# Performance work log

Measured on AMD Instinct MI355X. Metric: run time of the kernel, lower is better.

Reference implementation:

```python
import jax, jax.numpy as jnp
import numpy as np
from jax import lax

DROP_PROB = 0.1
BLOCK_SIZE = 7
B, C, H, W = 64, 256, 56, 56
HM, WM = H - (BLOCK_SIZE - 1), W - (BLOCK_SIZE - 1)


def setup_inputs() -> dict:
    key = jax.random.key(0)
    k1, k2 = jax.random.split(key)
    x = jax.random.normal(k1, (B, C, H, W), dtype=jnp.float32)
    mask_u = jax.random.uniform(k2, (B, C, HM, WM), dtype=jnp.float32)
    return {"x": x, "mask_u": mask_u}


def reference(x, mask_u):
    bs = BLOCK_SIZE
    feat = x.shape[2]
    # gamma as in _compute_gamma
    gamma = DROP_PROB / bs**2 * feat**2 / (feat - bs + 1) ** 2
    # Bernoulli(gamma) sample, deterministic given mask_u
    mask = (mask_u < gamma).astype(x.dtype)  # (B,C,HM,WM)
    # The nonzero/scatter block expansion in the original is exactly a
    # stride-1 max-pool with a bs x bs window and (bs-1, bs-1) zero padding,
    # producing the (B,C,H,W) padded dropped-region mask.
    blocked = lax.reduce_window(
        mask, 0.0, lax.max,
        window_dimensions=(1, 1, bs, bs),
        window_strides=(1, 1, 1, 1),
        padding=((0, 0), (0, 0), (bs - 1, bs - 1), (bs - 1, bs - 1)),
    )
    block_mask = 1.0 - blocked  # (B,C,H,W)
    scale = block_mask.size / block_mask.sum()
    return x * block_mask * scale
```

## Files before the change

kernel.cpp:

```cpp
#include <hip/hip_runtime.h>


#define BB 64
#define CC 256
#define HH 56
#define WW 56
#define HMM 50
#define WMM 50
#define BS 7

static constexpr unsigned int NPLANE = BB * CC;
static constexpr unsigned int NTOT   = BB * CC * HH * WW;
static constexpr unsigned int NV     = NTOT / 4;

__global__ void __launch_bounds__(256) dropblock_mask_kernel(
    const float* __restrict__ mask_u,
    unsigned long long* __restrict__ rowmask,
    unsigned int* __restrict__ plane_cnt,
    float gamma)
{
    const unsigned int wid   = threadIdx.x >> 6;
    const unsigned int lane  = threadIdx.x & 63u;
    const unsigned int plane = blockIdx.x * 4u + wid;
    const float* mu = mask_u + (size_t)plane * (HMM * WMM);

    unsigned long long my_d = 0ull;

    #pragma unroll
    for (int i = 0; i < HMM; ++i) {
        float v = (lane < WMM) ? mu[i * WMM + lane] : 1.0f;
        unsigned long long m = __ballot(v < gamma);
        unsigned long long d = m | (m << 1);
        d |= d << 2;
        d |= d << 3;
        if (lane == (unsigned)i) my_d = d;
    }

    unsigned long long blocked = my_d;
    blocked |= __shfl_up(blocked, 1, 64);
    blocked |= __shfl_up(blocked, 2, 64);
    blocked |= __shfl_up(blocked, 3, 64);

    if (lane < HH) rowmask[plane * HH + lane] = blocked;

    unsigned int cnt = __popcll(blocked);
    #pragma unroll
    for (int off = 32; off > 0; off >>= 1)
        cnt += __shfl_down(cnt, off, 64);
    if (lane == 0) plane_cnt[plane] = cnt;
}

__global__ void __launch_bounds__(1024) dropblock_scale_kernel(
    const unsigned int* __restrict__ plane_cnt,
    float* __restrict__ scale_out)
{
    __shared__ unsigned int ssum[16];
    const unsigned int t = threadIdx.x;

    const uint4* pc4 = reinterpret_cast<const uint4*>(plane_cnt);
    uint4 a = pc4[t];
    uint4 b = pc4[t + 1024];
    uint4 c = pc4[t + 2048];
    uint4 d = pc4[t + 3072];
    unsigned int s = a.x + a.y + a.z + a.w
                   + b.x + b.y + b.z + b.w
                   + c.x + c.y + c.z + c.w
                   + d.x + d.y + d.z + d.w;

    #pragma unroll
    for (int off = 32; off > 0; off >>= 1)
        s += __shfl_down(s, off, 64);
    if ((t & 63u) == 0u) ssum[t >> 6] = s;
    __syncthreads();

    if (t < 16) {
        unsigned int v = ssum[t];
        #pragma unroll
        for (int off = 8; off > 0; off >>= 1)
            v += __shfl_down(v, off, 64);
        if (t == 0) {
            *scale_out = (float)NTOT / (float)(NTOT - v);
        }
    }
}

__global__ void __launch_bounds__(256) dropblock_apply_kernel(
    const float* __restrict__ x,
    const unsigned long long* __restrict__ rowmask,
    const float* __restrict__ scale_ptr,
    float* __restrict__ out)
{
    unsigned int idx = blockIdx.x * 256u + threadIdx.x;
    if (idx >= NV) return;

    const float scale = *scale_ptr;

    unsigned int plane = idx / (HH * WW / 4);
    unsigned int rem   = idx - plane * (HH * WW / 4);
    unsigned int row   = rem / (WW / 4);
    unsigned int colv  = rem - row * (WW / 4);
    unsigned int col   = colv * 4;

    unsigned long long rm = rowmask[plane * HH + row];
    float4 xv = reinterpret_cast<const float4*>(x)[idx];
    float4 o;
    o.x = ((rm >> (col + 0)) & 1ull) ? 0.0f : xv.x * scale;
    o.y = ((rm >> (col + 1)) & 1ull) ? 0.0f : xv.y * scale;
    o.z = ((rm >> (col + 2)) & 1ull) ? 0.0f : xv.z * scale;
    o.w = ((rm >> (col + 3)) & 1ull) ? 0.0f : xv.w * scale;
    reinterpret_cast<float4*>(out)[idx] = o;
}

extern "C" void kernel_launch(void* const* d_in, const int* in_sizes, int n_in,
                              void* d_out, int out_size, void* d_ws, size_t ws_size,
                              hipStream_t stream) {
    const float* x      = (const float*)d_in[0];
    const float* mask_u = (const float*)d_in[1];
    float* out          = (float*)d_out;

    float* scale_ws             = (float*)d_ws;
    unsigned int* plane_cnt     = (unsigned int*)((char*)d_ws + 64);
    unsigned long long* rowmask = (unsigned long long*)((char*)d_ws + 65600);

    const double gd = 0.1 / ((double)BS * BS) * ((double)HH * HH) /
                      (((double)HH - BS + 1.0) * ((double)HH - BS + 1.0));
    const float gamma = (float)gd;

    dropblock_mask_kernel<<<NPLANE / 4, 256, 0, stream>>>(
        mask_u, rowmask, plane_cnt, gamma);

    dropblock_scale_kernel<<<1, 1024, 0, stream>>>(plane_cnt, scale_ws);

    dropblock_apply_kernel<<<(NV + 255u) / 256u, 256, 0, stream>>>(
        x, rowmask, scale_ws, out);
}
```

Measured before the change: 454.8 us.

## Stage mask_u through LDS with coalesced float4 prefetch, 16 planes per block

The mask kernel now loads four planes at a time into shared memory using coalesced float4 loads and register double-buffering. The next group of four planes is prefetched while the current one is processed with ballots. Each block handles 16 planes and writes one per-block count, so the scale kernel reduces 1024 values instead of 16384. This replaces strided 50-float row loads with fully vectorized streaming, at the cost of higher register and LDS use per block and lower parallelism in the mask kernel.

Result: faster. 440.5 us (-3.1%).

```diff
diff --git a/kernel.cpp b/kernel.cpp
--- a/kernel.cpp
+++ b/kernel.cpp
@@ -9,78 +9,114 @@
 #define WMM 50
 #define BS 7
 
-static constexpr unsigned int NPLANE = BB * CC;
-static constexpr unsigned int NTOT   = BB * CC * HH * WW;
-static constexpr unsigned int NV     = NTOT / 4;
+static constexpr unsigned int NPLANE  = BB * CC;
+static constexpr unsigned int NTOT    = BB * CC * HH * WW;
+static constexpr unsigned int NV      = NTOT / 4;
+static constexpr unsigned int PLANEF  = HMM * WMM;
+static constexpr unsigned int PLANE4  = PLANEF / 4;
+static constexpr unsigned int MGRID   = 1024;
+static constexpr unsigned int MPPB    = 16;
+static constexpr unsigned int MROUNDS = 4;
+static constexpr unsigned int R4CNT   = 4 * PLANE4;
+
+typedef float f32x4 __attribute__((ext_vector_type(4)));
 
 __global__ void __launch_bounds__(256) dropblock_mask_kernel(
     const float* __restrict__ mask_u,
     unsigned long long* __restrict__ rowmask,
-    unsigned int* __restrict__ plane_cnt,
+    unsigned int* __restrict__ block_cnt,
     float gamma)
 {
-    const unsigned int wid   = threadIdx.x >> 6;
-    const unsigned int lane  = threadIdx.x & 63u;
-    const unsigned int plane = blockIdx.x * 4u + wid;
-    const float* mu = mask_u + (size_t)plane * (HMM * WMM);
+    const unsigned int tid  = threadIdx.x;
+    const unsigned int wid  = tid >> 6;
+    const unsigned int lane = tid & 63u;
+    const unsigned int b    = blockIdx.x;
 
-    unsigned long long my_d = 0ull;
+    __shared__ float4 lds4[R4CNT];
+    __shared__ unsigned int csh[4];
+    const float* lds = reinterpret_cast<const float*>(lds4);
 
+    const float4* base = reinterpret_cast<const float4*>(mask_u)
+                       + (size_t)b * (MPPB * PLANE4);
+
+    float4 pf[10];
     #pragma unroll
-    for (int i = 0; i < HMM; ++i) {
-        float v = (lane < WMM) ? mu[i * WMM + lane] : 1.0f;
-        unsigned long long m = __ballot(v < gamma);
-        unsigned long long d = m | (m << 1);
-        d |= d << 2;
-        d |= d << 3;
-        if (lane == (unsigned)i) my_d = d;
+    for (unsigned int s = 0; s < 10; ++s) {
+        unsigned int i = tid + s * 256u;
+        pf[s] = (i < R4CNT) ? base[i] : make_float4(0.f, 0.f, 0.f, 0.f);
     }
 
-    unsigned long long blocked = my_d;
-    blocked |= __shfl_up(blocked, 1, 64);
-    blocked |= __shfl_up(blocked, 2, 64);
-    blocked |= __shfl_up(blocked, 3, 64);
+    unsigned int wcnt = 0;
 
-    if (lane < HH) rowmask[plane * HH + lane] = blocked;
+    for (unsigned int r = 0; r < MROUNDS; ++r) {
+        #pragma unroll
+        for (unsigned int s = 0; s < 10; ++s) {
+            unsigned int i = tid + s * 256u;
+            if (i < R4CNT) lds4[i] = pf[s];
+        }
+        __syncthreads();
 
-    unsigned int cnt = __popcll(blocked);
-    #pragma unroll
-    for (int off = 32; off > 0; off >>= 1)
-        cnt += __shfl_down(cnt, off, 64);
-    if (lane == 0) plane_cnt[plane] = cnt;
+        if (r + 1 < MROUNDS) {
+            const float4* src = base + (r + 1) * R4CNT;
+            #pragma unroll
+            for (unsigned int s = 0; s < 10; ++s) {
+                unsigned int i = tid + s * 256u;
+                pf[s] = (i < R4CNT) ? src[i] : make_float4(0.f, 0.f, 0.f, 0.f);
+            }
+        }
+
+        const float* mu = lds + wid * PLANEF;
+        unsigned long long my_d = 0ull;
+        #pragma unroll
+        for (int i = 0; i < HMM; ++i) {
+            float v = (lane < WMM) ? mu[i * WMM + lane] : 1.0f;
+            unsigned long long m = __ballot(v < gamma);
+            unsigned long long d = m | (m << 1);
+            d |= d << 2;
+            d |= d << 3;
+            if (lane == (unsigned)i) my_d = d;
+        }
+        unsigned long long blocked = my_d;
+        blocked |= __shfl_up(blocked, 1, 64);
+        blocked |= __shfl_up(blocked, 2, 64);
+        blocked |= __shfl_up(blocked, 3, 64);
+
+        const unsigned int plane = b * MPPB + r * 4u + wid;
+        if (lane < HH) rowmask[plane * HH + lane] = blocked;
+
+        unsigned int c = __popcll(blocked);
+        #pragma unroll
+        for (int off = 32; off > 0; off >>= 1)
+            c += __shfl_down(c, off, 64);
+        if (lane == 0) wcnt += c;
+
+        __syncthreads();
+    }
+
+    if (lane == 0) csh[wid] = wcnt;
+    __syncthreads();
+    if (tid == 0) block_cnt[b] = csh[0] + csh[1] + csh[2] + csh[3];
 }
 
-__global__ void __launch_bounds__(1024) dropblock_scale_kernel(
-    const unsigned int* __restrict__ plane_cnt,
+__global__ void __launch_bounds__(256) dropblock_scale_kernel(
+    const unsigned int* __restrict__ block_cnt,
     float* __restrict__ scale_out)
 {
-    __shared__ unsigned int ssum[16];
+    __shared__ unsigned int ssum[4];
     const unsigned int t = threadIdx.x;
 
-    const uint4* pc4 = reinterpret_cast<const uint4*>(plane_cnt);
-    uint4 a = pc4[t];
-    uint4 b = pc4[t + 1024];
-    uint4 c = pc4[t + 2048];
-    uint4 d = pc4[t + 3072];
-    unsigned int s = a.x + a.y + a.z + a.w
-                   + b.x + b.y + b.z + b.w
-                   + c.x + c.y + c.z + c.w
-                   + d.x + d.y + d.z + d.w;
-
+    const uint4* c4 = reinterpret_cast<const uint4*>(block_cnt);
+    uint4 v = c4[t];
+    unsigned int s = v.x + v.y + v.z + v.w;
     #pragma unroll
     for (int off = 32; off > 0; off >>= 1)
         s += __shfl_down(s, off, 64);
     if ((t & 63u) == 0u) ssum[t >> 6] = s;
     __syncthreads();
 
-    if (t < 16) {
-        unsigned int v = ssum[t];
-        #pragma unroll
-        for (int off = 8; off > 0; off >>= 1)
-            v += __shfl_down(v, off, 64);
-        if (t == 0) {
-            *scale_out = (float)NTOT / (float)(NTOT - v);
-        }
+    if (t == 0) {
+        unsigned int tot = ssum[0] + ssum[1] + ssum[2] + ssum[3];
+        *scale_out = (float)NTOT / (float)(NTOT - tot);
     }
 }
 
@@ -119,17 +155,17 @@
     float* out          = (float*)d_out;
 
     float* scale_ws             = (float*)d_ws;
-    unsigned int* plane_cnt     = (unsigned int*)((char*)d_ws + 64);
-    unsigned long long* rowmask = (unsigned long long*)((char*)d_ws + 65600);
+    unsigned int* block_cnt     = (unsigned int*)((char*)d_ws + 64);
+    unsigned long long* rowmask = (unsigned long long*)((char*)d_ws + 8192);
 
     const double gd = 0.1 / ((double)BS * BS) * ((double)HH * HH) /
                       (((double)HH - BS + 1.0) * ((double)HH - BS + 1.0));
     const float gamma = (float)gd;
 
-    dropblock_mask_kernel<<<NPLANE / 4, 256, 0, stream>>>(
-        mask_u, rowmask, plane_cnt, gamma);
+    dropblock_mask_kernel<<<MGRID, 256, 0, stream>>>(
+        mask_u, rowmask, block_cnt, gamma);
 
-    dropblock_scale_kernel<<<1, 1024, 0, stream>>>(plane_cnt, scale_ws);
+    dropblock_scale_kernel<<<1, 256, 0, stream>>>(block_cnt, scale_ws);
 
     dropblock_apply_kernel<<<(NV + 255u) / 256u, 256, 0, stream>>>(
         x, rowmask, scale_ws, out);
```
